# Optimization experiments

Measured on AMD Instinct MI355X. Metric: run time of the kernel, lower is better.

Reference implementation:

```python
import jax, jax.numpy as jnp
import numpy as np

N = 50000
E = 500000
IN_DIM = 384
HID = 256
HEADS = 4
OUT_DIM = 128
NEG_SLOPE = 0.2


def _glorot(key, shape):
    fan_in, fan_out = shape[0], shape[-1]
    lim = jnp.sqrt(6.0 / (fan_in + fan_out))
    return jax.random.uniform(key, shape, jnp.float32, -lim, lim)


def setup_inputs() -> dict:
    key = jax.random.key(0)
    ks = jax.random.split(key, 16)
    x = jax.random.normal(ks[0], (N, IN_DIM), jnp.float32)
    node_attr = jax.random.normal(ks[1], (N, 2), jnp.float32)
    edge_index = jax.random.randint(ks[2], (2, E), 0, N, jnp.int64)
    return {
        "x": x,
        "node_attr": node_attr,
        "edge_index": edge_index,
        # node_encoder: Linear(386 -> 384)
        "enc_W": _glorot(ks[3], (IN_DIM + 2, IN_DIM)),
        "enc_b": jnp.zeros((IN_DIM,), jnp.float32),
        # gat1: 384 -> 4 heads x 256, concat
        "W1": _glorot(ks[4], (IN_DIM, HEADS * HID)),
        "a_src1": _glorot(ks[5], (HEADS, HID)),
        "a_dst1": _glorot(ks[6], (HEADS, HID)),
        "b1": jnp.zeros((HEADS * HID,), jnp.float32),
        # gat2: 1024 -> 1 head x 128, mean (concat=False)
        "W2": _glorot(ks[7], (HEADS * HID, OUT_DIM)),
        "a_src2": _glorot(ks[8], (1, OUT_DIM)),
        "a_dst2": _glorot(ks[9], (1, OUT_DIM)),
        "b2": jnp.zeros((OUT_DIM,), jnp.float32),
    }


def gat_conv(x, src, dst, W, a_src, a_dst, bias, heads, out_ch, concat):
    # x: [N, F]; src/dst: [E'] (self-loops already included)
    n = x.shape[0]
    h = (x @ W).reshape(n, heads, out_ch)          # [N, H, C]
    alpha_s = jnp.einsum('nhc,hc->nh', h, a_src)   # [N, H]
    alpha_d = jnp.einsum('nhc,hc->nh', h, a_dst)
    e = alpha_s[src] + alpha_d[dst]                # [E', H]
    e = jnp.where(e >= 0, e, NEG_SLOPE * e)        # LeakyReLU(0.2)
    # segment softmax over incoming edges of each destination node
    m = jax.ops.segment_max(e, dst, num_segments=n)
    e = jnp.exp(e - m[dst])
    denom = jax.ops.segment_sum(e, dst, num_segments=n)
    alpha = e / (denom[dst] + 1e-16)               # [E', H]
    msg = h[src] * alpha[:, :, None]               # [E', H, C]
    out = jax.ops.segment_sum(msg, dst, num_segments=n)  # [N, H, C]
    out = out.reshape(n, heads * out_ch) if concat else out.mean(axis=1)
    return out + bias


def reference(x, node_attr, edge_index, enc_W, enc_b,
              W1, a_src1, a_dst1, b1, W2, a_src2, a_dst2, b2):
    n = x.shape[0]
    # node encoder on [x ; node_attr]
    h = jnp.concatenate([x, node_attr], axis=-1) @ enc_W + enc_b
    # add self-loops once (PyG GATConv default add_self_loops=True)
    loop = jnp.arange(n, dtype=edge_index.dtype)
    src = jnp.concatenate([edge_index[0], loop])
    dst = jnp.concatenate([edge_index[1], loop])
    h = gat_conv(h, src, dst, W1, a_src1, a_dst1, b1, HEADS, HID, True)
    h = jax.nn.elu(h)
    out = gat_conv(h, src, dst, W2, a_src2, a_dst2, b2, 1, OUT_DIM, False)
    return out
```

## Files before the change

kernel.cpp:

```cpp
#include <hip/hip_runtime.h>
#include <hip/hip_bf16.h>
#include <type_traits>


#define NN 50000
#define NE 500000
#define EP (NE + NN)

typedef __hip_bfloat16 bf16;
typedef short short8 __attribute__((ext_vector_type(8)));
typedef __bf16 bf16x8 __attribute__((ext_vector_type(8)));
typedef float f32x4 __attribute__((ext_vector_type(4)));

__device__ __forceinline__ float b2f(bf16 v) { return __bfloat162float(v); }
__device__ __forceinline__ bf16  f2b(float v) { return __float2bfloat16(v); }
__device__ __forceinline__ unsigned short f2bu(float v) {
  bf16 b = __float2bfloat16(v);
  return *reinterpret_cast<unsigned short*>(&b);
}

__device__ __forceinline__ float ldf(const void* p, size_t i, bool f32) {
  return f32 ? ((const float*)p)[i] : b2f(((const bf16*)p)[i]);
}

__device__ __forceinline__ float bflo(unsigned u) { return __uint_as_float(u << 16); }
__device__ __forceinline__ float bfhi(unsigned u) { return __uint_as_float(u & 0xffff0000u); }

__device__ __forceinline__ float leaky(float v) { return v >= 0.f ? v : 0.2f * v; }

__global__ void k_detect_edge(const unsigned int* __restrict__ w, unsigned int* __restrict__ flag) {
  unsigned int acc = 0;
  for (int i = blockIdx.x * 256 + threadIdx.x; i < NE; i += gridDim.x * 256)
    acc |= w[2 * i + 1];
  if (acc) atomicOr(flag, 1u);
}

__global__ void k_detect_f32(const unsigned int* __restrict__ w, unsigned int* __restrict__ flag) {
  unsigned int acc = 0;
  for (int i = blockIdx.x * 256 + threadIdx.x; i < (1 << 20); i += gridDim.x * 256) {
    unsigned int e = (w[i] >> 7) & 0xFF;
    if (e > 0xA0) acc = 1;
  }
  if (acc) atomicOr(flag, 1u);
}

__global__ void k_convert(const int* __restrict__ ei, const unsigned int* __restrict__ flag,
                          int* __restrict__ esrc, int* __restrict__ edst,
                          int* __restrict__ deg) {
  int e = blockIdx.x * 256 + threadIdx.x;
  if (e >= EP) return;
  int s, d;
  if (e < NE) {
    if (*flag) { s = ei[e]; d = ei[NE + e]; }
    else { const long long* e64 = (const long long*)ei; s = (int)e64[e]; d = (int)e64[NE + e]; }
    s = min(max(s, 0), NN - 1);
    d = min(max(d, 0), NN - 1);
  } else {
    s = d = e - NE;
  }
  esrc[e] = s;
  edst[e] = d;
  atomicAdd(&deg[d], 1);
}

__global__ void k_pack_cat(const void* __restrict__ x, const void* __restrict__ na,
                           bf16* __restrict__ catp, const unsigned int* __restrict__ fflag) {
  const bool f32 = (*fflag != 0);
  for (int i = blockIdx.x * 256 + threadIdx.x; i < NN * 416; i += gridDim.x * 256) {
    int n = i / 416, c = i - n * 416;
    float v = 0.f;
    if (c < 384)      v = ldf(x,  (size_t)n * 384 + c, f32);
    else if (c < 386) v = ldf(na, (size_t)n * 2 + (c - 384), f32);
    catp[i] = f2b(v);
  }
}

__global__ void k_pack_w(const void* __restrict__ W, bf16* __restrict__ Wp,
                         int K, int Kpad, int N, const unsigned int* __restrict__ fflag) {
  const bool f32 = (*fflag != 0);
  int total = Kpad * N;
  for (int i = blockIdx.x * 256 + threadIdx.x; i < total; i += gridDim.x * 256) {
    int kb = i / (N * 32);
    int rem = i - kb * N * 32;
    int n = rem >> 5, kk = rem & 31;
    int k = kb * 32 + kk;
    float v = (k < K) ? ldf(W, (size_t)k * N + n, f32) : 0.f;
    Wp[i] = f2b(v);
  }
}

template<bool ADD_BIAS, typename CT>
__global__ __launch_bounds__(256) void gemm_mfma(
    const bf16* __restrict__ A, int lda,
    const bf16* __restrict__ Bp,
    const void* __restrict__ bias,
    CT* __restrict__ C,
    int M, int N, int K,
    const unsigned int* __restrict__ fflag) {
  const bool f32 = ADD_BIAS ? (*fflag != 0) : false;
  __shared__ short As[128 * 40];
  __shared__ short Bs[128 * 40];
  const int t = threadIdx.x;
  const int lane = t & 63, wave = t >> 6;
  const int wm = wave & 1, wn = wave >> 1;
  const int quad = lane >> 4, l15 = lane & 15;
  const int m0 = blockIdx.x * 128, n0 = blockIdx.y * 128;

  f32x4 acc[4][4];
#pragma unroll
  for (int i = 0; i < 4; ++i)
#pragma unroll
    for (int j = 0; j < 4; ++j) acc[i][j] = (f32x4){0.f, 0.f, 0.f, 0.f};

  for (int k0 = 0; k0 < K; k0 += 32) {
#pragma unroll
    for (int i = 0; i < 2; ++i) {
      int c = t + i * 256;
      int row = c >> 2, koff = (c & 3) * 8;
      int gm = min(m0 + row, M - 1);
      const short* src = (const short*)A + (size_t)gm * lda + k0 + koff;
      *(short8*)&As[row * 40 + koff] = *(const short8*)src;
    }
    {
      const short* base = (const short*)Bp + ((size_t)(k0 >> 5) * N + n0) * 32;
#pragma unroll
      for (int i = 0; i < 2; ++i) {
        int c = t + i * 256;
        int nl = c >> 2, koff = (c & 3) * 8;
        *(short8*)&Bs[nl * 40 + koff] = *(const short8*)(base + nl * 32 + koff);
      }
    }
    __syncthreads();
    bf16x8 af[4], bfr[4];
#pragma unroll
    for (int mi = 0; mi < 4; ++mi)
      af[mi] = *reinterpret_cast<const bf16x8*>(&As[(wm * 64 + mi * 16 + l15) * 40 + quad * 8]);
#pragma unroll
    for (int ni = 0; ni < 4; ++ni)
      bfr[ni] = *reinterpret_cast<const bf16x8*>(&Bs[(wn * 64 + ni * 16 + l15) * 40 + quad * 8]);
#pragma unroll
    for (int mi = 0; mi < 4; ++mi)
#pragma unroll
      for (int ni = 0; ni < 4; ++ni)
        acc[mi][ni] = __builtin_amdgcn_mfma_f32_16x16x32_bf16(af[mi], bfr[ni], acc[mi][ni], 0, 0, 0);
    __syncthreads();
  }

#pragma unroll
  for (int mi = 0; mi < 4; ++mi) {
#pragma unroll
    for (int ni = 0; ni < 4; ++ni) {
      const int gn = n0 + wn * 64 + ni * 16 + l15;
      float bv = ADD_BIAS ? ldf(bias, gn, f32) : 0.f;
#pragma unroll
      for (int r = 0; r < 4; ++r) {
        const int gm = m0 + wm * 64 + mi * 16 + quad * 4 + r;
        if (gm < M) {
          float v = acc[mi][ni][r] + bv;
          if constexpr (std::is_same<CT, float>::value)
            C[(size_t)gm * N + gn] = v;
          else
            C[(size_t)gm * N + gn] = f2b(v);
        }
      }
    }
  }
}

__global__ void k_alpha1(const bf16* __restrict__ h1, const void* __restrict__ a_src,
                         const void* __restrict__ a_dst,
                         float* __restrict__ as, float* __restrict__ ad,
                         const unsigned int* __restrict__ fflag) {
  const bool f32 = (*fflag != 0);
  int n = blockIdx.x, t = threadIdx.x;
  const bf16* hrow = h1 + (size_t)n * 1024;
  float s[4], d[4];
#pragma unroll
  for (int j = 0; j < 4; ++j) {
    float v = b2f(hrow[j * 256 + t]);
    s[j] = v * ldf(a_src, j * 256 + t, f32);
    d[j] = v * ldf(a_dst, j * 256 + t, f32);
  }
#pragma unroll
  for (int off = 32; off > 0; off >>= 1) {
#pragma unroll
    for (int j = 0; j < 4; ++j) {
      s[j] += __shfl_down(s[j], off, 64);
      d[j] += __shfl_down(d[j], off, 64);
    }
  }
  __shared__ float ls[4][4], ld_[4][4];
  int w = t >> 6;
  if ((t & 63) == 0) {
#pragma unroll
    for (int j = 0; j < 4; ++j) { ls[w][j] = s[j]; ld_[w][j] = d[j]; }
  }
  __syncthreads();
  if (t < 4) {
    as[n * 4 + t] = ls[0][t] + ls[1][t] + ls[2][t] + ls[3][t];
    ad[n * 4 + t] = ld_[0][t] + ld_[1][t] + ld_[2][t] + ld_[3][t];
  }
}

__global__ void k_alpha2(const float* __restrict__ h2, const void* __restrict__ a_src,
                         const void* __restrict__ a_dst,
                         float* __restrict__ as, float* __restrict__ ad,
                         const unsigned int* __restrict__ fflag) {
  const bool f32 = (*fflag != 0);
  int n = blockIdx.x, t = threadIdx.x;
  float v = h2[(size_t)n * 128 + t];
  float s = v * ldf(a_src, t, f32);
  float d = v * ldf(a_dst, t, f32);
#pragma unroll
  for (int off = 32; off > 0; off >>= 1) {
    s += __shfl_down(s, off, 64);
    d += __shfl_down(d, off, 64);
  }
  __shared__ float ls[2], ld_[2];
  if ((t & 63) == 0) { ls[t >> 6] = s; ld_[t >> 6] = d; }
  __syncthreads();
  if (t == 0) { as[n] = ls[0] + ls[1]; ad[n] = ld_[0] + ld_[1]; }
}

#define SCAN_B 512
#define SCAN_NB ((NN + SCAN_B - 1) / SCAN_B)

__global__ __launch_bounds__(SCAN_B) void k_scan1(const int* __restrict__ deg,
                                                  int* __restrict__ row_ptr,
                                                  int* __restrict__ partial) {
  int b = blockIdx.x, t = threadIdx.x;
  int i = b * SCAN_B + t;
  int v = (i < NN) ? deg[i] : 0;
  int lane = t & 63, w = t >> 6;
  int x = v;
#pragma unroll
  for (int off = 1; off < 64; off <<= 1) {
    int y = __shfl_up(x, off, 64);
    if (lane >= off) x += y;
  }
  __shared__ int ws[8];
  if (lane == 63) ws[w] = x;
  __syncthreads();
  if (t == 0) {
    int run = 0;
#pragma unroll
    for (int j = 0; j < 8; ++j) { int tmp = ws[j]; ws[j] = run; run += tmp; }
    partial[b] = run;
  }
  __syncthreads();
  int excl = x - v + ws[w];
  if (i < NN) row_ptr[i] = excl;
}

__global__ void k_scan2(int* __restrict__ partial, int* __restrict__ row_ptr) {
  if (blockIdx.x == 0 && threadIdx.x == 0) {
    int run = 0;
    for (int j = 0; j < SCAN_NB; ++j) { int tmp = partial[j]; partial[j] = run; run += tmp; }
    row_ptr[NN] = run;
  }
}

__global__ __launch_bounds__(SCAN_B) void k_scan3(const int* __restrict__ partial,
                                                  int* __restrict__ row_ptr,
                                                  int* __restrict__ cursor) {
  int b = blockIdx.x, t = threadIdx.x;
  int i = b * SCAN_B + t;
  if (i < NN) {
    int v = row_ptr[i] + partial[b];
    row_ptr[i] = v;
    cursor[i] = v;
  }
}

__global__ void k_scatter(const int* __restrict__ esrc, const int* __restrict__ edst,
                          int* __restrict__ cursor, int* __restrict__ csr) {
  int e = blockIdx.x * 256 + threadIdx.x;
  if (e >= EP) return;
  int pos = atomicAdd(&cursor[edst[e]], 1);
  pos = min(max(pos, 0), EP - 1);
  csr[pos] = esrc[e];
}

__global__ __launch_bounds__(256) void k_agg1(
    const int* __restrict__ csr, const int* __restrict__ row_ptr,
    const float* __restrict__ as1, const float* __restrict__ ad1,
    const bf16* __restrict__ h1, const void* __restrict__ b1,
    bf16* __restrict__ act1, const unsigned int* __restrict__ fflag) {
  const bool f32 = (*fflag != 0);
  const int n = blockIdx.x, t = threadIdx.x;
  const int w = t >> 6, l = t & 63;
  const int start = row_ptr[n], end = row_ptr[n + 1];
  const float adn = ad1[n * 4 + w];
  const unsigned* hb = (const unsigned*)h1;
  const int coff = w * 128 + l * 2;

  float a0 = 0.f, a1 = 0.f, a2 = 0.f, a3 = 0.f, densum = 0.f;

  int idx = start;
  for (; idx + 4 <= end; idx += 4) {
    int s0 = csr[idx], s1 = csr[idx + 1], s2 = csr[idx + 2], s3 = csr[idx + 3];
    uint2 w0 = *(const uint2*)(hb + (size_t)s0 * 512 + coff);
    uint2 w1 = *(const uint2*)(hb + (size_t)s1 * 512 + coff);
    uint2 w2 = *(const uint2*)(hb + (size_t)s2 * 512 + coff);
    uint2 w3 = *(const uint2*)(hb + (size_t)s3 * 512 + coff);
    float p0 = __expf(leaky(as1[s0 * 4 + w] + adn));
    float p1 = __expf(leaky(as1[s1 * 4 + w] + adn));
    float p2 = __expf(leaky(as1[s2 * 4 + w] + adn));
    float p3 = __expf(leaky(as1[s3 * 4 + w] + adn));
    densum += (p0 + p1) + (p2 + p3);
    a0 = fmaf(bflo(w0.x), p0, a0); a1 = fmaf(bfhi(w0.x), p0, a1);
    a2 = fmaf(bflo(w0.y), p0, a2); a3 = fmaf(bfhi(w0.y), p0, a3);
    a0 = fmaf(bflo(w1.x), p1, a0); a1 = fmaf(bfhi(w1.x), p1, a1);
    a2 = fmaf(bflo(w1.y), p1, a2); a3 = fmaf(bfhi(w1.y), p1, a3);
    a0 = fmaf(bflo(w2.x), p2, a0); a1 = fmaf(bfhi(w2.x), p2, a1);
    a2 = fmaf(bflo(w2.y), p2, a2); a3 = fmaf(bfhi(w2.y), p2, a3);
    a0 = fmaf(bflo(w3.x), p3, a0); a1 = fmaf(bfhi(w3.x), p3, a1);
    a2 = fmaf(bflo(w3.y), p3, a2); a3 = fmaf(bfhi(w3.y), p3, a3);
  }
  for (; idx < end; ++idx) {
    int s0 = csr[idx];
    uint2 w0 = *(const uint2*)(hb + (size_t)s0 * 512 + coff);
    float p0 = __expf(leaky(as1[s0 * 4 + w] + adn));
    densum += p0;
    a0 = fmaf(bflo(w0.x), p0, a0); a1 = fmaf(bfhi(w0.x), p0, a1);
    a2 = fmaf(bflo(w0.y), p0, a2); a3 = fmaf(bfhi(w0.y), p0, a3);
  }

  const float inv = 1.f / (densum + 1e-16f);
  const int col = w * 256 + l * 4;
  float v0 = a0 * inv + ldf(b1, col + 0, f32);
  float v1 = a1 * inv + ldf(b1, col + 1, f32);
  float v2 = a2 * inv + ldf(b1, col + 2, f32);
  float v3 = a3 * inv + ldf(b1, col + 3, f32);
  v0 = v0 > 0.f ? v0 : expm1f(v0);
  v1 = v1 > 0.f ? v1 : expm1f(v1);
  v2 = v2 > 0.f ? v2 : expm1f(v2);
  v3 = v3 > 0.f ? v3 : expm1f(v3);
  ushort2 o0, o1;
  o0.x = f2bu(v0); o0.y = f2bu(v1);
  o1.x = f2bu(v2); o1.y = f2bu(v3);
  ushort2* orow = (ushort2*)((unsigned short*)act1 + (size_t)n * 1024 + col);
  orow[0] = o0; orow[1] = o1;
}

__global__ __launch_bounds__(256) void k_agg2(
    const int* __restrict__ csr, const int* __restrict__ row_ptr,
    const float* __restrict__ as2, const float* __restrict__ ad2,
    const float* __restrict__ h2, const void* __restrict__ b2v,
    float* __restrict__ out, const unsigned int* __restrict__ fflag) {
  const bool f32 = (*fflag != 0);
  const int n = blockIdx.x, t = threadIdx.x;
  const int w = t >> 6, l = t & 63;
  const int start = row_ptr[n], end = row_ptr[n + 1];
  const float adn = ad2[n];
  float ax = 0.f, ay = 0.f, densum = 0.f;

  for (int idx = start + w; idx < end; idx += 4) {
    int s = csr[idx];
    const float2 hv = *(const float2*)(h2 + (size_t)s * 128 + l * 2);
    float pe = __expf(leaky(as2[s] + adn));
    densum += pe;
    ax = fmaf(hv.x, pe, ax);
    ay = fmaf(hv.y, pe, ay);
  }

  __shared__ float2 red[4][64];
  __shared__ float dsum[4];
  if (w > 0) {
    red[w][l] = make_float2(ax, ay);
    if (l == 0) dsum[w] = densum;
  }
  __syncthreads();
  if (w == 0) {
#pragma unroll
    for (int j = 1; j < 4; ++j) {
      float2 o = red[j][l];
      ax += o.x; ay += o.y;
    }
    densum += dsum[1] + dsum[2] + dsum[3];
    const float inv = 1.f / (densum + 1e-16f);
    float* orow = out + (size_t)n * 128 + l * 2;
    orow[0] = ax * inv + ldf(b2v, l * 2 + 0, f32);
    orow[1] = ay * inv + ldf(b2v, l * 2 + 1, f32);
  }
}

extern "C" void kernel_launch(void* const* d_in, const int* in_sizes, int n_in,
                              void* d_out, int out_size, void* d_ws, size_t ws_size,
                              hipStream_t stream) {
  const void* x       = d_in[0];
  const void* na      = d_in[1];
  const int*  ei      = (const int*)d_in[2];
  const void* enc_W   = d_in[3];
  const void* enc_b   = d_in[4];
  const void* W1      = d_in[5];
  const void* a_src1  = d_in[6];
  const void* a_dst1  = d_in[7];
  const void* b1      = d_in[8];
  const void* W2      = d_in[9];
  const void* a_src2  = d_in[10];
  const void* a_dst2  = d_in[11];
  const void* b2      = d_in[12];
  float* out = (float*)d_out;

  size_t off = 0;
  char* ws = (char*)d_ws;
  auto alloc = [&](size_t bytes) -> void* {
    void* p = ws + off;
    off += (bytes + 255) & ~(size_t)255;
    return p;
  };
  bf16*  h1      = (bf16*)alloc((size_t)NN * 1024 * 2);
  bf16*  act1    = (bf16*)alloc((size_t)NN * 1024 * 2);
  bf16*  catp    = act1;
  float* h0f     = (float*)alloc((size_t)NN * 384 * 2);
  bf16*  h0      = (bf16*)h0f;
  float* h2      = h0f;
  bf16*  encWp   = (bf16*)alloc((size_t)416 * 384 * 2);
  bf16*  W1p     = (bf16*)alloc((size_t)384 * 1024 * 2);
  bf16*  W2p     = (bf16*)alloc((size_t)1024 * 128 * 2);
  int*   esrc    = (int*)alloc((size_t)EP * 4);
  int*   edst    = (int*)alloc((size_t)EP * 4);
  unsigned int* eflag = (unsigned int*)alloc(4);
  unsigned int* fflag = (unsigned int*)alloc(4);
  int*   csr     = (int*)alloc((size_t)EP * 4);
  float* as1     = (float*)alloc((size_t)NN * 4 * 4);
  float* ad1     = (float*)alloc((size_t)NN * 4 * 4);
  float* as2     = (float*)alloc((size_t)NN * 4);
  float* ad2     = (float*)alloc((size_t)NN * 4);
  int*   deg     = (int*)alloc((size_t)NN * 4);
  int*   row_ptr = (int*)alloc((size_t)(NN + 1) * 4);
  int*   cursor  = (int*)alloc((size_t)NN * 4);
  int*   partial = (int*)alloc((size_t)SCAN_NB * 4);
  (void)ws_size; (void)in_sizes; (void)n_in; (void)out_size;

  (void)hipMemsetAsync(eflag, 0, 4,              stream);
  (void)hipMemsetAsync(fflag, 0, 4,              stream);
  (void)hipMemsetAsync(deg,   0, (size_t)NN * 4, stream);

  const int EB = (EP + 255) / 256;
  const int MB = (NN + 127) / 128;

  k_detect_edge<<<512, 256, 0, stream>>>((const unsigned int*)ei, eflag);
  k_detect_f32<<<512, 256, 0, stream>>>((const unsigned int*)x, fflag);

  k_convert<<<EB, 256, 0, stream>>>(ei, eflag, esrc, edst, deg);
  k_scan1<<<SCAN_NB, SCAN_B, 0, stream>>>(deg, row_ptr, partial);
  k_scan2<<<1, 64, 0, stream>>>(partial, row_ptr);
  k_scan3<<<SCAN_NB, SCAN_B, 0, stream>>>(partial, row_ptr, cursor);
  k_scatter<<<EB, 256, 0, stream>>>(esrc, edst, cursor, csr);

  k_pack_cat<<<8192, 256, 0, stream>>>(x, na, catp, fflag);
  k_pack_w<<<1024, 256, 0, stream>>>(enc_W, encWp, 386, 416, 384, fflag);
  k_pack_w<<<1024, 256, 0, stream>>>(W1, W1p, 384, 384, 1024, fflag);
  k_pack_w<<<1024, 256, 0, stream>>>(W2, W2p, 1024, 1024, 128, fflag);

  gemm_mfma<true, bf16><<<dim3(MB, 3), 256, 0, stream>>>(catp, 416, encWp, enc_b, h0, NN, 384, 416, fflag);
  gemm_mfma<false, bf16><<<dim3(MB, 8), 256, 0, stream>>>(h0, 384, W1p, nullptr, h1, NN, 1024, 384, fflag);

  k_alpha1<<<NN, 256, 0, stream>>>(h1, a_src1, a_dst1, as1, ad1, fflag);
  k_agg1<<<NN, 256, 0, stream>>>(csr, row_ptr, as1, ad1, h1, b1, act1, fflag);

  gemm_mfma<false, float><<<dim3(MB, 1), 256, 0, stream>>>(act1, 1024, W2p, nullptr, h2, NN, 128, 1024, fflag);

  k_alpha2<<<NN, 128, 0, stream>>>(h2, a_src2, a_dst2, as2, ad2, fflag);
  k_agg2<<<NN, 256, 0, stream>>>(csr, row_ptr, as2, ad2, h2, b2, out, fflag);
}
```

Measured before the change: 793.5 us.

## Fold node encoder into first GAT projection by precomputing combined weight

Since the encoder and the GAT1 projection are consecutive linear maps with no nonlinearity between them, the code precomputes enc_W @ W1 (386x1024) with a small GEMM written directly in packed B layout, and folds enc_b @ W1 into a bias vector. The input is then multiplied once by this combined weight (K=416, N=1024). This drops the 50000x384 intermediate write and read plus the separate encoder GEMM. In exchange it adds a tiny GEMM, a serial bias kernel and a memset, and rounding changes because the combined weight is stored in bf16.

```diff
diff --git a/kernel.cpp b/kernel.cpp
--- a/kernel.cpp
+++ b/kernel.cpp
@@ -75,6 +75,13 @@
   }
 }
 
+__global__ void k_pack_rows(const void* __restrict__ src, bf16* __restrict__ dst,
+                            int total, const unsigned int* __restrict__ fflag) {
+  const bool f32 = (*fflag != 0);
+  for (int i = blockIdx.x * 256 + threadIdx.x; i < total; i += gridDim.x * 256)
+    dst[i] = f2b(ldf(src, i, f32));
+}
+
 __global__ void k_pack_w(const void* __restrict__ W, bf16* __restrict__ Wp,
                          int K, int Kpad, int N, const unsigned int* __restrict__ fflag) {
   const bool f32 = (*fflag != 0);
@@ -89,7 +96,18 @@
   }
 }
 
-template<bool ADD_BIAS, typename CT>
+__global__ void k_bvec(const void* __restrict__ enc_b, const void* __restrict__ W1,
+                       float* __restrict__ bvec, const unsigned int* __restrict__ fflag) {
+  const bool f32 = (*fflag != 0);
+  int n = blockIdx.x * 256 + threadIdx.x;
+  if (n >= 1024) return;
+  float acc = 0.f;
+  for (int k = 0; k < 384; ++k)
+    acc = fmaf(ldf(enc_b, k, f32), ldf(W1, (size_t)k * 1024 + n, f32), acc);
+  bvec[n] = acc;
+}
+
+template<bool ADD_BIAS, bool BIAS_F32, bool PACK_OUT, typename CT>
 __global__ __launch_bounds__(256) void gemm_mfma(
     const bf16* __restrict__ A, int lda,
     const bf16* __restrict__ Bp,
@@ -97,7 +115,7 @@
     CT* __restrict__ C,
     int M, int N, int K,
     const unsigned int* __restrict__ fflag) {
-  const bool f32 = ADD_BIAS ? (*fflag != 0) : false;
+  const bool f32 = (ADD_BIAS && !BIAS_F32) ? (*fflag != 0) : true;
   __shared__ short As[128 * 40];
   __shared__ short Bs[128 * 40];
   const int t = threadIdx.x;
@@ -151,16 +169,19 @@
 #pragma unroll
     for (int ni = 0; ni < 4; ++ni) {
       const int gn = n0 + wn * 64 + ni * 16 + l15;
-      float bv = ADD_BIAS ? ldf(bias, gn, f32) : 0.f;
+      float bv = 0.f;
+      if (ADD_BIAS) bv = BIAS_F32 ? ((const float*)bias)[gn] : ldf(bias, gn, f32);
 #pragma unroll
       for (int r = 0; r < 4; ++r) {
         const int gm = m0 + wm * 64 + mi * 16 + quad * 4 + r;
         if (gm < M) {
           float v = acc[mi][ni][r] + bv;
+          size_t ci = PACK_OUT ? (((size_t)(gm >> 5) * N + gn) * 32 + (gm & 31))
+                               : ((size_t)gm * N + gn);
           if constexpr (std::is_same<CT, float>::value)
-            C[(size_t)gm * N + gn] = v;
+            C[ci] = v;
           else
-            C[(size_t)gm * N + gn] = f2b(v);
+            C[ci] = f2b(v);
         }
       }
     }
@@ -412,13 +433,13 @@
   };
   bf16*  h1      = (bf16*)alloc((size_t)NN * 1024 * 2);
   bf16*  act1    = (bf16*)alloc((size_t)NN * 1024 * 2);
-  bf16*  catp    = act1;
-  float* h0f     = (float*)alloc((size_t)NN * 384 * 2);
-  bf16*  h0      = (bf16*)h0f;
-  float* h2      = h0f;
-  bf16*  encWp   = (bf16*)alloc((size_t)416 * 384 * 2);
+  float* h2      = (float*)alloc((size_t)NN * 128 * 4);
+  bf16*  catp    = (bf16*)alloc((size_t)NN * 416 * 2);
   bf16*  W1p     = (bf16*)alloc((size_t)384 * 1024 * 2);
   bf16*  W2p     = (bf16*)alloc((size_t)1024 * 128 * 2);
+  bf16*  encA    = (bf16*)alloc((size_t)386 * 384 * 2);
+  bf16*  Wcp     = (bf16*)alloc((size_t)416 * 1024 * 2);
+  float* bvec    = (float*)alloc((size_t)1024 * 4);
   int*   esrc    = (int*)alloc((size_t)EP * 4);
   int*   edst    = (int*)alloc((size_t)EP * 4);
   unsigned int* eflag = (unsigned int*)alloc(4);
@@ -434,9 +455,10 @@
   int*   partial = (int*)alloc((size_t)SCAN_NB * 4);
   (void)ws_size; (void)in_sizes; (void)n_in; (void)out_size;
 
-  (void)hipMemsetAsync(eflag, 0, 4,              stream);
-  (void)hipMemsetAsync(fflag, 0, 4,              stream);
-  (void)hipMemsetAsync(deg,   0, (size_t)NN * 4, stream);
+  (void)hipMemsetAsync(eflag, 0, 4,                      stream);
+  (void)hipMemsetAsync(fflag, 0, 4,                      stream);
+  (void)hipMemsetAsync(deg,   0, (size_t)NN * 4,         stream);
+  (void)hipMemsetAsync(Wcp,   0, (size_t)416 * 1024 * 2, stream);
 
   const int EB = (EP + 255) / 256;
   const int MB = (NN + 127) / 128;
@@ -451,17 +473,21 @@
   k_scatter<<<EB, 256, 0, stream>>>(esrc, edst, cursor, csr);
 
   k_pack_cat<<<8192, 256, 0, stream>>>(x, na, catp, fflag);
-  k_pack_w<<<1024, 256, 0, stream>>>(enc_W, encWp, 386, 416, 384, fflag);
   k_pack_w<<<1024, 256, 0, stream>>>(W1, W1p, 384, 384, 1024, fflag);
   k_pack_w<<<1024, 256, 0, stream>>>(W2, W2p, 1024, 1024, 128, fflag);
-
-  gemm_mfma<true, bf16><<<dim3(MB, 3), 256, 0, stream>>>(catp, 416, encWp, enc_b, h0, NN, 384, 416, fflag);
-  gemm_mfma<false, bf16><<<dim3(MB, 8), 256, 0, stream>>>(h0, 384, W1p, nullptr, h1, NN, 1024, 384, fflag);
+  k_pack_rows<<<256, 256, 0, stream>>>(enc_W, encA, 386 * 384, fflag);
+  k_bvec<<<4, 256, 0, stream>>>(enc_b, W1, bvec, fflag);
+  gemm_mfma<false, false, true, bf16><<<dim3(4, 8), 256, 0, stream>>>(
+      encA, 384, W1p, nullptr, Wcp, 386, 1024, 384, fflag);
+
+  gemm_mfma<true, true, false, bf16><<<dim3(MB, 8), 256, 0, stream>>>(
+      catp, 416, Wcp, bvec, h1, NN, 1024, 416, fflag);
 
   k_alpha1<<<NN, 256, 0, stream>>>(h1, a_src1, a_dst1, as1, ad1, fflag);
   k_agg1<<<NN, 256, 0, stream>>>(csr, row_ptr, as1, ad1, h1, b1, act1, fflag);
 
-  gemm_mfma<false, float><<<dim3(MB, 1), 256, 0, stream>>>(act1, 1024, W2p, nullptr, h2, NN, 128, 1024, fflag);
+  gemm_mfma<false, false, false, float><<<dim3(MB, 1), 256, 0, stream>>>(
+      act1, 1024, W2p, nullptr, h2, NN, 128, 1024, fflag);
 
   k_alpha2<<<NN, 128, 0, stream>>>(h2, a_src2, a_dst2, as2, ad2, fflag);
   k_agg2<<<NN, 256, 0, stream>>>(csr, row_ptr, as2, ad2, h2, b2, out, fflag);
```

Result: slower. 843.5 us (+6.3%).

## Fuse attention-logit projections into GEMM epilogues and store layer-2 features in bf16

Applied to the files above, without the earlier changes.

The separate alpha1/alpha2 kernels are removed. Their dot products with a_src/a_dst are now computed in the MFMA GEMM epilogue from the accumulators, reduced within each 16-lane group and atomically added into zeroed buffers. h2 is stored as bf16 instead of fp32, and agg2 is rewritten to read packed bf16 pairs with 8 groups of 32 threads. The cat-packing kernel is vectorised to four elements per thread. These changes drop two passes over h1/h2 and halve the gather traffic in agg2, at the cost of float atomics, extra memsets, and reduced precision for h2.

```diff
diff --git a/kernel.cpp b/kernel.cpp
--- a/kernel.cpp
+++ b/kernel.cpp
@@ -66,12 +66,28 @@
 __global__ void k_pack_cat(const void* __restrict__ x, const void* __restrict__ na,
                            bf16* __restrict__ catp, const unsigned int* __restrict__ fflag) {
   const bool f32 = (*fflag != 0);
-  for (int i = blockIdx.x * 256 + threadIdx.x; i < NN * 416; i += gridDim.x * 256) {
-    int n = i / 416, c = i - n * 416;
-    float v = 0.f;
-    if (c < 384)      v = ldf(x,  (size_t)n * 384 + c, f32);
-    else if (c < 386) v = ldf(na, (size_t)n * 2 + (c - 384), f32);
-    catp[i] = f2b(v);
+  const int total = NN * 104;
+  for (int g = blockIdx.x * 256 + threadIdx.x; g < total; g += gridDim.x * 256) {
+    int n = g / 104, r = g - n * 104;
+    int c = r * 4;
+    float v0 = 0.f, v1 = 0.f, v2 = 0.f, v3 = 0.f;
+    if (c < 384) {
+      if (f32) {
+        const float4 f = *(const float4*)((const float*)x + (size_t)n * 384 + c);
+        v0 = f.x; v1 = f.y; v2 = f.z; v3 = f.w;
+      } else {
+        const bf16* xb = (const bf16*)x + (size_t)n * 384 + c;
+        v0 = b2f(xb[0]); v1 = b2f(xb[1]); v2 = b2f(xb[2]); v3 = b2f(xb[3]);
+      }
+    } else if (c == 384) {
+      v0 = ldf(na, (size_t)n * 2 + 0, f32);
+      v1 = ldf(na, (size_t)n * 2 + 1, f32);
+    }
+    ushort2 o0, o1;
+    o0.x = f2bu(v0); o0.y = f2bu(v1);
+    o1.x = f2bu(v2); o1.y = f2bu(v3);
+    ushort2* dst = (ushort2*)((unsigned short*)catp + (size_t)n * 416 + c);
+    dst[0] = o0; dst[1] = o1;
   }
 }
 
@@ -89,15 +105,17 @@
   }
 }
 
-template<bool ADD_BIAS, typename CT>
+template<bool ADD_BIAS, bool ALPHA, int NH, typename CT>
 __global__ __launch_bounds__(256) void gemm_mfma(
     const bf16* __restrict__ A, int lda,
     const bf16* __restrict__ Bp,
     const void* __restrict__ bias,
+    const void* __restrict__ a_srcp, const void* __restrict__ a_dstp,
+    float* __restrict__ as_out, float* __restrict__ ad_out,
     CT* __restrict__ C,
     int M, int N, int K,
     const unsigned int* __restrict__ fflag) {
-  const bool f32 = ADD_BIAS ? (*fflag != 0) : false;
+  const bool xf32 = (ADD_BIAS || ALPHA) ? (*fflag != 0) : false;
   __shared__ short As[128 * 40];
   __shared__ short Bs[128 * 40];
   const int t = threadIdx.x;
@@ -151,7 +169,7 @@
 #pragma unroll
     for (int ni = 0; ni < 4; ++ni) {
       const int gn = n0 + wn * 64 + ni * 16 + l15;
-      float bv = ADD_BIAS ? ldf(bias, gn, f32) : 0.f;
+      float bv = ADD_BIAS ? ldf(bias, gn, xf32) : 0.f;
 #pragma unroll
       for (int r = 0; r < 4; ++r) {
         const int gm = m0 + wm * 64 + mi * 16 + quad * 4 + r;
@@ -165,61 +183,42 @@
       }
     }
   }
-}
-
-__global__ void k_alpha1(const bf16* __restrict__ h1, const void* __restrict__ a_src,
-                         const void* __restrict__ a_dst,
-                         float* __restrict__ as, float* __restrict__ ad,
-                         const unsigned int* __restrict__ fflag) {
-  const bool f32 = (*fflag != 0);
-  int n = blockIdx.x, t = threadIdx.x;
-  const bf16* hrow = h1 + (size_t)n * 1024;
-  float s[4], d[4];
-#pragma unroll
-  for (int j = 0; j < 4; ++j) {
-    float v = b2f(hrow[j * 256 + t]);
-    s[j] = v * ldf(a_src, j * 256 + t, f32);
-    d[j] = v * ldf(a_dst, j * 256 + t, f32);
-  }
-#pragma unroll
-  for (int off = 32; off > 0; off >>= 1) {
-#pragma unroll
-    for (int j = 0; j < 4; ++j) {
-      s[j] += __shfl_down(s[j], off, 64);
-      d[j] += __shfl_down(d[j], off, 64);
-    }
-  }
-  __shared__ float ls[4][4], ld_[4][4];
-  int w = t >> 6;
-  if ((t & 63) == 0) {
-#pragma unroll
-    for (int j = 0; j < 4; ++j) { ls[w][j] = s[j]; ld_[w][j] = d[j]; }
-  }
-  __syncthreads();
-  if (t < 4) {
-    as[n * 4 + t] = ls[0][t] + ls[1][t] + ls[2][t] + ls[3][t];
-    ad[n * 4 + t] = ld_[0][t] + ld_[1][t] + ld_[2][t] + ld_[3][t];
-  }
-}
-
-__global__ void k_alpha2(const float* __restrict__ h2, const void* __restrict__ a_src,
-                         const void* __restrict__ a_dst,
-                         float* __restrict__ as, float* __restrict__ ad,
-                         const unsigned int* __restrict__ fflag) {
-  const bool f32 = (*fflag != 0);
-  int n = blockIdx.x, t = threadIdx.x;
-  float v = h2[(size_t)n * 128 + t];
-  float s = v * ldf(a_src, t, f32);
-  float d = v * ldf(a_dst, t, f32);
-#pragma unroll
-  for (int off = 32; off > 0; off >>= 1) {
-    s += __shfl_down(s, off, 64);
-    d += __shfl_down(d, off, 64);
-  }
-  __shared__ float ls[2], ld_[2];
-  if ((t & 63) == 0) { ls[t >> 6] = s; ld_[t >> 6] = d; }
-  __syncthreads();
-  if (t == 0) { as[n] = ls[0] + ls[1]; ad[n] = ld_[0] + ld_[1]; }
+
+  if (ALPHA) {
+    float avs[4], avd[4];
+#pragma unroll
+    for (int ni = 0; ni < 4; ++ni) {
+      const int gn = n0 + wn * 64 + ni * 16 + l15;
+      avs[ni] = ldf(a_srcp, gn, xf32);
+      avd[ni] = ldf(a_dstp, gn, xf32);
+    }
+    const int head = (n0 + wn * 64) >> 8;
+#pragma unroll
+    for (int mi = 0; mi < 4; ++mi) {
+#pragma unroll
+      for (int r = 0; r < 4; ++r) {
+        float ps = 0.f, pd = 0.f;
+#pragma unroll
+        for (int ni = 0; ni < 4; ++ni) {
+          const float v = acc[mi][ni][r];
+          ps = fmaf(v, avs[ni], ps);
+          pd = fmaf(v, avd[ni], pd);
+        }
+#pragma unroll
+        for (int off = 8; off > 0; off >>= 1) {
+          ps += __shfl_down(ps, off, 16);
+          pd += __shfl_down(pd, off, 16);
+        }
+        if (l15 == 0) {
+          const int gm = m0 + wm * 64 + mi * 16 + quad * 4 + r;
+          if (gm < M) {
+            atomicAdd(&as_out[gm * NH + head], ps);
+            atomicAdd(&ad_out[gm * NH + head], pd);
+          }
+        }
+      }
+    }
+  }
 }
 
 #define SCAN_B 512
@@ -346,42 +345,45 @@
 __global__ __launch_bounds__(256) void k_agg2(
     const int* __restrict__ csr, const int* __restrict__ row_ptr,
     const float* __restrict__ as2, const float* __restrict__ ad2,
-    const float* __restrict__ h2, const void* __restrict__ b2v,
+    const bf16* __restrict__ h2, const void* __restrict__ b2v,
     float* __restrict__ out, const unsigned int* __restrict__ fflag) {
   const bool f32 = (*fflag != 0);
   const int n = blockIdx.x, t = threadIdx.x;
-  const int w = t >> 6, l = t & 63;
+  const int g = t >> 5, tc = t & 31;
   const int start = row_ptr[n], end = row_ptr[n + 1];
   const float adn = ad2[n];
-  float ax = 0.f, ay = 0.f, densum = 0.f;
-
-  for (int idx = start + w; idx < end; idx += 4) {
+  const unsigned* hb = (const unsigned*)h2;
+  float a0 = 0.f, a1 = 0.f, a2 = 0.f, a3 = 0.f, densum = 0.f;
+
+  for (int idx = start + g; idx < end; idx += 8) {
     int s = csr[idx];
-    const float2 hv = *(const float2*)(h2 + (size_t)s * 128 + l * 2);
+    const uint2 w = *(const uint2*)(hb + (size_t)s * 64 + tc * 2);
     float pe = __expf(leaky(as2[s] + adn));
     densum += pe;
-    ax = fmaf(hv.x, pe, ax);
-    ay = fmaf(hv.y, pe, ay);
-  }
-
-  __shared__ float2 red[4][64];
-  __shared__ float dsum[4];
-  if (w > 0) {
-    red[w][l] = make_float2(ax, ay);
-    if (l == 0) dsum[w] = densum;
+    a0 = fmaf(bflo(w.x), pe, a0); a1 = fmaf(bfhi(w.x), pe, a1);
+    a2 = fmaf(bflo(w.y), pe, a2); a3 = fmaf(bfhi(w.y), pe, a3);
+  }
+
+  __shared__ float4 red[8][32];
+  __shared__ float dsum[8];
+  if (g > 0) {
+    red[g][tc] = make_float4(a0, a1, a2, a3);
+    if (tc == 0) dsum[g] = densum;
   }
   __syncthreads();
-  if (w == 0) {
-#pragma unroll
-    for (int j = 1; j < 4; ++j) {
-      float2 o = red[j][l];
-      ax += o.x; ay += o.y;
-    }
-    densum += dsum[1] + dsum[2] + dsum[3];
+  if (g == 0) {
+#pragma unroll
+    for (int j = 1; j < 8; ++j) {
+      const float4 o = red[j][tc];
+      a0 += o.x; a1 += o.y; a2 += o.z; a3 += o.w;
+      densum += dsum[j];
+    }
     const float inv = 1.f / (densum + 1e-16f);
-    float* orow = out + (size_t)n * 128 + l * 2;
-    orow[0] = ax * inv + ldf(b2v, l * 2 + 0, f32);
-    orow[1] = ay * inv + ldf(b2v, l * 2 + 1, f32);
+    float* orow = out + (size_t)n * 128 + tc * 4;
+    orow[0] = a0 * inv + ldf(b2v, tc * 4 + 0, f32);
+    orow[1] = a1 * inv + ldf(b2v, tc * 4 + 1, f32);
+    orow[2] = a2 * inv + ldf(b2v, tc * 4 + 2, f32);
+    orow[3] = a3 * inv + ldf(b2v, tc * 4 + 3, f32);
   }
 }
 
@@ -413,9 +415,8 @@
   bf16*  h1      = (bf16*)alloc((size_t)NN * 1024 * 2);
   bf16*  act1    = (bf16*)alloc((size_t)NN * 1024 * 2);
   bf16*  catp    = act1;
-  float* h0f     = (float*)alloc((size_t)NN * 384 * 2);
-  bf16*  h0      = (bf16*)h0f;
-  float* h2      = h0f;
+  bf16*  h0      = (bf16*)alloc((size_t)NN * 384 * 2);
+  bf16*  h2      = (bf16*)alloc((size_t)NN * 128 * 2);
   bf16*  encWp   = (bf16*)alloc((size_t)416 * 384 * 2);
   bf16*  W1p     = (bf16*)alloc((size_t)384 * 1024 * 2);
   bf16*  W2p     = (bf16*)alloc((size_t)1024 * 128 * 2);
@@ -434,9 +435,13 @@
   int*   partial = (int*)alloc((size_t)SCAN_NB * 4);
   (void)ws_size; (void)in_sizes; (void)n_in; (void)out_size;
 
-  (void)hipMemsetAsync(eflag, 0, 4,              stream);
-  (void)hipMemsetAsync(fflag, 0, 4,              stream);
-  (void)hipMemsetAsync(deg,   0, (size_t)NN * 4, stream);
+  (void)hipMemsetAsync(eflag, 0, 4,               stream);
+  (void)hipMemsetAsync(fflag, 0, 4,               stream);
+  (void)hipMemsetAsync(deg,   0, (size_t)NN * 4,  stream);
+  (void)hipMemsetAsync(as1,   0, (size_t)NN * 16, stream);
+  (void)hipMemsetAsync(ad1,   0, (size_t)NN * 16, stream);
+  (void)hipMemsetAsync(as2,   0, (size_t)NN * 4,  stream);
+  (void)hipMemsetAsync(ad2,   0, (size_t)NN * 4,  stream);
 
   const int EB = (EP + 255) / 256;
   const int MB = (NN + 127) / 128;
@@ -455,14 +460,18 @@
   k_pack_w<<<1024, 256, 0, stream>>>(W1, W1p, 384, 384, 1024, fflag);
   k_pack_w<<<1024, 256, 0, stream>>>(W2, W2p, 1024, 1024, 128, fflag);
 
-  gemm_mfma<true, bf16><<<dim3(MB, 3), 256, 0, stream>>>(catp, 416, encWp, enc_b, h0, NN, 384, 416, fflag);
-  gemm_mfma<false, bf16><<<dim3(MB, 8), 256, 0, stream>>>(h0, 384, W1p, nullptr, h1, NN, 1024, 384, fflag);
-
-  k_alpha1<<<NN, 256, 0, stream>>>(h1, a_src1, a_dst1, as1, ad1, fflag);
+  gemm_mfma<true, false, 1, bf16><<<dim3(MB, 3), 256, 0, stream>>>(
+      catp, 416, encWp, enc_b, nullptr, nullptr, nullptr, nullptr,
+      h0, NN, 384, 416, fflag);
+  gemm_mfma<false, true, 4, bf16><<<dim3(MB, 8), 256, 0, stream>>>(
+      h0, 384, W1p, nullptr, a_src1, a_dst1, as1, ad1,
+      h1, NN, 1024, 384, fflag);
+
   k_agg1<<<NN, 256, 0, stream>>>(csr, row_ptr, as1, ad1, h1, b1, act1, fflag);
 
-  gemm_mfma<false, float><<<dim3(MB, 1), 256, 0, stream>>>(act1, 1024, W2p, nullptr, h2, NN, 128, 1024, fflag);
-
-  k_alpha2<<<NN, 128, 0, stream>>>(h2, a_src2, a_dst2, as2, ad2, fflag);
+  gemm_mfma<false, true, 1, bf16><<<dim3(MB, 1), 256, 0, stream>>>(
+      act1, 1024, W2p, nullptr, a_src2, a_dst2, as2, ad2,
+      h2, NN, 128, 1024, fflag);
+
   k_agg2<<<NN, 256, 0, stream>>>(csr, row_ptr, as2, ad2, h2, b2, out, fflag);
 }
```

Result: faster. 711.8 us (-10.3%).
